# Kernel optimization log

Measured on AMD Instinct MI355X. Metric: run time of the kernel, lower is better.

The kernel has to match this reference:

```python
import jax, jax.numpy as jnp
import numpy as np

TABLE = 4194304   # maxGridFeatId[-1]
D = 4             # eachGridFeatDim
L = 6             # gridFeatLevelCnt (code indexes sigma1..sigma6)
DIR = 16          # in_dim_dir
H = 64            # hidden_dim_color
B, N = 16384, 128


def _linear_init(key, fan_in, fan_out):
    # matches torch nn.Linear default U(-1/sqrt(fan_in), 1/sqrt(fan_in))
    s = 1.0 / np.sqrt(fan_in)
    kw, kb = jax.random.split(key)
    W = jax.random.uniform(kw, (fan_in, fan_out), minval=-s, maxval=s, dtype=jnp.float32)
    b = jax.random.uniform(kb, (fan_out,), minval=-s, maxval=s, dtype=jnp.float32)
    return W, b


def setup_inputs() -> dict:
    key = jax.random.key(0)
    ks = jax.random.split(key, 6)
    x = jax.random.randint(ks[0], (B, N, L), 0, TABLE)
    d = jax.random.normal(ks[1], (B, DIR), dtype=jnp.float32)
    gridWeight = jax.random.uniform(ks[2], (TABLE, D), dtype=jnp.float32)  # torch.rand
    in0 = DIR + L * (D - 1)  # 16 + 18 = 34
    W0, b0 = _linear_init(ks[3], in0, H)
    W1, b1 = _linear_init(ks[4], H, H)
    W2, b2 = _linear_init(ks[5], H, 3)
    return dict(x=x, d=d, gridWeight=gridWeight, W0=W0, b0=b0, W1=W1, b1=b1, W2=W2, b2=b2)


def reference(x, d, gridWeight, W0, b0, W1, b1, W2, b2):
    Bv, Nv, Lv = x.shape
    Dv = gridWeight.shape[-1]
    # embedding gather: (B, N, L, D); same memory order as torch reshape(B, N*L, D)
    feat = gridWeight[x]
    # per-level densities, clipped then multiplied (prod over the 6 levels)
    sig = jnp.clip(feat[..., 0], 0.0, 1.0)                 # (B, N, L)
    sigma0 = jnp.prod(sig, axis=-1, keepdims=True) + 1e-4  # (B, N, 1)
    sigma = sigma0 / jnp.max(sigma0, axis=1, keepdims=True)
    # geometric features: (B, N, L*(D-1))
    geo = feat[..., 1:].reshape(Bv, Nv, Lv * (Dv - 1))
    h = jnp.concatenate([jnp.broadcast_to(d[:, None, :], (Bv, Nv, d.shape[-1])), geo], axis=-1)
    h = jax.nn.relu(h @ W0 + b0)
    h = jax.nn.relu(h @ W1 + b1)
    color = jax.nn.sigmoid(h @ W2 + b2)                    # (B, N, 3)
    # alpha compositing: NOTE original does torch.cumprod(..., dim=2) on a
    # (B, N, 1) tensor, i.e. cumprod over a size-1 axis == identity. Faithful.
    alpha = 1.0 - sigma
    transparentBefore = jnp.concatenate(
        [jnp.ones((Bv, 1, 1), dtype=sigma.dtype), alpha[:, :-1]], axis=1)
    colorWeight0 = transparentBefore * sigma               # (B, N, 1)
    colorOut = colorWeight0 * color                        # (B, N, 3)
    return sigma, jnp.sum(colorOut, axis=1)                # (B,N,1), (B,3)
```

## Files before the change

kernel.cpp:

```cpp
#include <hip/hip_runtime.h>
#include <math.h>


typedef short bf16x8 __attribute__((ext_vector_type(8)));
typedef float floatx4 __attribute__((ext_vector_type(4)));

__device__ inline unsigned short f2b(float f) {
    union { float f; unsigned u; } v; v.f = f;
    unsigned r = v.u + 0x7FFF + ((v.u >> 16) & 1);
    return (unsigned short)(r >> 16);
}

__global__ void build_frags(const float* __restrict__ W0,
                            const float* __restrict__ W1,
                            const float* __restrict__ W2,
                            unsigned short* __restrict__ wsf) {
    int tid = blockIdx.x * blockDim.x + threadIdx.x;
    if (tid >= 7168) return;
    int lane, j, k, n;
    float val;
    if (tid < 2048) {
        int f = tid >> 9, r = tid & 511; lane = r >> 3; j = r & 7;
        k = ((lane >> 4) * 8) + j;
        n = f * 16 + (lane & 15);
        val = (k < 18) ? W0[(16 + k) * 64 + n] : 0.0f;
    } else if (tid < 6144) {
        int e = tid - 2048;
        int f = e >> 9, r = e & 511; lane = r >> 3; j = r & 7;
        int ks = f >> 2, nt = f & 3;
        k = ks * 32 + ((lane >> 4) * 8) + j;
        n = nt * 16 + (lane & 15);
        val = W1[k * 64 + n];
    } else {
        int e = tid - 6144;
        int f = e >> 9, r = e & 511; lane = r >> 3; j = r & 7;
        k = f * 32 + ((lane >> 4) * 8) + j;
        n = lane & 15;
        val = (n < 3) ? W2[k * 3 + n] : 0.0f;
    }
    wsf[tid] = f2b(val);
}

__global__ __launch_bounds__(512, 4) void surf_main(
    const int*   __restrict__ x,
    const float* __restrict__ dvec,
    const float* __restrict__ gw,
    const float* __restrict__ W0,
    const float* __restrict__ b0,
    const float* __restrict__ b1,
    const float* __restrict__ b2,
    const unsigned short* __restrict__ wsf,
    float* __restrict__ out_sigma,
    float* __restrict__ out_color)
{
    const int b    = blockIdx.x;
    const int t    = threadIdx.x;
    const int lane = t & 63;
    const int w    = t >> 6;
    const int l15  = lane & 15;
    const int quad = lane >> 4;

    __shared__ unsigned short A0[128 * 40];
    __shared__ unsigned short H1[128 * 72];
    __shared__ float s_sigl[768];
    __shared__ float s_dirW[64];
    __shared__ float s_wmax[2];
    __shared__ float s_cw[128];
    __shared__ float s_part[8 * 16];

    bf16x8 bw0[4], bw1[8];
    #pragma unroll
    for (int i = 0; i < 4; ++i) bw0[i] = *(const bf16x8*)(wsf + i * 512 + lane * 8);
    #pragma unroll
    for (int i = 0; i < 8; ++i) bw1[i] = *(const bf16x8*)(wsf + 2048 + i * 512 + lane * 8);

    #pragma unroll
    for (int e0 = 0; e0 < 768; e0 += 512) {
        int e = e0 + t;
        if (e < 768) {
            int xv = x[(size_t)b * 768 + e];
            int point = e / 6;
            int level = e - point * 6;
            float4 v = *(const float4*)(gw + (size_t)xv * 4);
            s_sigl[e] = fminf(fmaxf(v.x, 0.0f), 1.0f);
            unsigned short* a = A0 + point * 40 + level * 3;
            a[0] = f2b(v.y); a[1] = f2b(v.z); a[2] = f2b(v.w);
        }
    }
    if (t < 128) {
        unsigned short* a = A0 + t * 40;
        *(unsigned int*)(a + 18) = 0u;
        *(uint2*)(a + 20) = make_uint2(0u, 0u);
        *(uint2*)(a + 24) = make_uint2(0u, 0u);
        *(uint2*)(a + 28) = make_uint2(0u, 0u);
    }
    if (t < 64) {
        float acc = b0[t];
        const float* db = dvec + (size_t)b * 16;
        #pragma unroll
        for (int i = 0; i < 16; ++i) acc = fmaf(db[i], W0[i * 64 + t], acc);
        s_dirW[t] = acc;
    }
    __syncthreads();

    float sigma0 = 0.0f;
    if (t < 128) {
        float p = 1.0f;
        #pragma unroll
        for (int l = 0; l < 6; ++l) p *= s_sigl[t * 6 + l];
        sigma0 = p + 1e-4f;
        float m = sigma0;
        #pragma unroll
        for (int off = 32; off; off >>= 1) m = fmaxf(m, __shfl_xor(m, off));
        if (lane == 0) s_wmax[w] = m;
    }
    __syncthreads();
    if (t < 128) {
        float maxv  = fmaxf(s_wmax[0], s_wmax[1]);
        float sigma = sigma0 / maxv;
        out_sigma[(size_t)b * 128 + t] = sigma;
        float cw;
        if (t == 0) cw = sigma;
        else {
            float pp = 1.0f;
            #pragma unroll
            for (int l = 0; l < 6; ++l) pp *= s_sigl[(t - 1) * 6 + l];
            float sprev = (pp + 1e-4f) / maxv;
            cw = (1.0f - sprev) * sigma;
        }
        s_cw[t] = cw;
    }

    const int row = w * 16 + l15;
    bf16x8 a0 = *(const bf16x8*)(A0 + row * 40 + quad * 8);
    floatx4 acc0[4];
    #pragma unroll
    for (int nt = 0; nt < 4; ++nt) {
        float dw = s_dirW[nt * 16 + l15];
        acc0[nt] = (floatx4){dw, dw, dw, dw};
        acc0[nt] = __builtin_amdgcn_mfma_f32_16x16x32_bf16(a0, bw0[nt], acc0[nt], 0, 0, 0);
    }
    #pragma unroll
    for (int nt = 0; nt < 4; ++nt)
        #pragma unroll
        for (int r = 0; r < 4; ++r) {
            int pr = w * 16 + quad * 4 + r;
            H1[pr * 72 + nt * 16 + l15] = f2b(fmaxf(acc0[nt][r], 0.0f));
        }

    bf16x8 a1a = *(const bf16x8*)(H1 + row * 72 + quad * 8);
    bf16x8 a1b = *(const bf16x8*)(H1 + row * 72 + 32 + quad * 8);
    floatx4 acc1[4];
    #pragma unroll
    for (int nt = 0; nt < 4; ++nt) {
        float bb = b1[nt * 16 + l15];
        acc1[nt] = (floatx4){bb, bb, bb, bb};
        acc1[nt] = __builtin_amdgcn_mfma_f32_16x16x32_bf16(a1a, bw1[nt],     acc1[nt], 0, 0, 0);
        acc1[nt] = __builtin_amdgcn_mfma_f32_16x16x32_bf16(a1b, bw1[4 + nt], acc1[nt], 0, 0, 0);
    }
    #pragma unroll
    for (int nt = 0; nt < 4; ++nt)
        #pragma unroll
        for (int r = 0; r < 4; ++r) {
            int pr = w * 16 + quad * 4 + r;
            H1[pr * 72 + nt * 16 + l15] = f2b(fmaxf(acc1[nt][r], 0.0f));
        }

    bf16x8 bw2a = *(const bf16x8*)(wsf + 6144 + lane * 8);
    bf16x8 bw2b = *(const bf16x8*)(wsf + 6144 + 512 + lane * 8);
    bf16x8 a2a = *(const bf16x8*)(H1 + row * 72 + quad * 8);
    bf16x8 a2b = *(const bf16x8*)(H1 + row * 72 + 32 + quad * 8);
    float bias2 = (l15 < 3) ? b2[l15] : 0.0f;
    floatx4 acc2 = (floatx4){bias2, bias2, bias2, bias2};
    acc2 = __builtin_amdgcn_mfma_f32_16x16x32_bf16(a2a, bw2a, acc2, 0, 0, 0);
    acc2 = __builtin_amdgcn_mfma_f32_16x16x32_bf16(a2b, bw2b, acc2, 0, 0, 0);

    __syncthreads();
    float sum = 0.0f;
    #pragma unroll
    for (int r = 0; r < 4; ++r) {
        float col = 1.0f / (1.0f + __expf(-acc2[r]));
        float cw  = s_cw[w * 16 + quad * 4 + r];
        sum += cw * col;
    }
    sum += __shfl_xor(sum, 16);
    sum += __shfl_xor(sum, 32);
    if (lane < 16) s_part[w * 16 + lane] = sum;
    __syncthreads();
    if (t < 3) {
        float o = 0.0f;
        #pragma unroll
        for (int ww = 0; ww < 8; ++ww) o += s_part[ww * 16 + t];
        out_color[(size_t)b * 3 + t] = o;
    }
}

extern "C" void kernel_launch(void* const* d_in, const int* in_sizes, int n_in,
                              void* d_out, int out_size, void* d_ws, size_t ws_size,
                              hipStream_t stream) {
    const int*   x    = (const int*)d_in[0];
    const float* dvec = (const float*)d_in[1];
    const float* gw   = (const float*)d_in[2];
    const float* W0   = (const float*)d_in[3];
    const float* b0   = (const float*)d_in[4];
    const float* W1   = (const float*)d_in[5];
    const float* b1   = (const float*)d_in[6];
    const float* W2   = (const float*)d_in[7];
    const float* b2   = (const float*)d_in[8];

    const int B = in_sizes[1] / 16;
    float* out_sigma = (float*)d_out;
    float* out_color = (float*)d_out + (size_t)B * 128;
    unsigned short* wsf = (unsigned short*)d_ws;

    build_frags<<<14, 512, 0, stream>>>(W0, W1, W2, wsf);
    surf_main<<<B, 512, 0, stream>>>(x, dvec, gw, W0, b0, b1, b2, wsf,
                                     out_sigma, out_color);
}
```

Before: 336.5 us.

## Process several rays per block with software-pipelined gather prefetch

Each block now handles four rays in a loop instead of one, prefetching the next ray's grid gathers and the following ray's indices while the current ray's MLP runs. Weight fragments are staged once into shared memory per block rather than held in registers, which frees registers so launch bounds can ask for higher occupancy. The aim is to hide the random-gather latency and spread per-block setup over more rays. The cost is more shared-memory traffic for the weight fragments, extra syncs inside the loop, and a grid that is four times smaller.

Measured after the change: 391.2 us. 16.3% more time.

```diff
diff --git a/kernel.cpp b/kernel.cpp
--- a/kernel.cpp
+++ b/kernel.cpp
@@ -1,6 +1,8 @@
 #include <hip/hip_runtime.h>
 #include <math.h>
 
+
+#define RPB 4
 
 typedef short bf16x8 __attribute__((ext_vector_type(8)));
 typedef float floatx4 __attribute__((ext_vector_type(4)));
@@ -41,157 +43,200 @@
     wsf[tid] = f2b(val);
 }
 
-__global__ __launch_bounds__(512, 4) void surf_main(
+__global__ __launch_bounds__(512, 6) void surf_main(
     const int*   __restrict__ x,
     const float* __restrict__ dvec,
     const float* __restrict__ gw,
     const float* __restrict__ W0,
-    const float* __restrict__ b0,
-    const float* __restrict__ b1,
-    const float* __restrict__ b2,
+    const float* __restrict__ b0v,
+    const float* __restrict__ b1v,
+    const float* __restrict__ b2v,
     const unsigned short* __restrict__ wsf,
     float* __restrict__ out_sigma,
     float* __restrict__ out_color)
 {
-    const int b    = blockIdx.x;
     const int t    = threadIdx.x;
     const int lane = t & 63;
     const int w    = t >> 6;
     const int l15  = lane & 15;
     const int quad = lane >> 4;
 
-    __shared__ unsigned short A0[128 * 40];
-    __shared__ unsigned short H1[128 * 72];
+    __shared__ unsigned short UB[128 * 72];
+    __shared__ unsigned short WF[7168];
     __shared__ float s_sigl[768];
     __shared__ float s_dirW[64];
     __shared__ float s_wmax[2];
     __shared__ float s_cw[128];
-    __shared__ float s_part[8 * 16];
-
-    bf16x8 bw0[4], bw1[8];
+    __shared__ float s_part[128];
+
+    const size_t ray0 = (size_t)blockIdx.x * RPB;
+
+    {
+        const unsigned int* src = (const unsigned int*)wsf;
+        unsigned int* dst = (unsigned int*)WF;
+        #pragma unroll
+        for (int i = 0; i < 7; ++i) dst[t + i * 512] = src[t + i * 512];
+    }
+
+    float b1r[4];
     #pragma unroll
-    for (int i = 0; i < 4; ++i) bw0[i] = *(const bf16x8*)(wsf + i * 512 + lane * 8);
+    for (int nt = 0; nt < 4; ++nt) b1r[nt] = b1v[nt * 16 + l15];
+    const float b2r = (l15 < 3) ? b2v[l15] : 0.0f;
+
+    float dwAll[RPB];
+    if (t < 64) {
+        #pragma unroll
+        for (int r = 0; r < RPB; ++r) {
+            float acc = b0v[t];
+            const float* db = dvec + (ray0 + r) * 16;
+            #pragma unroll
+            for (int i = 0; i < 16; ++i) acc = fmaf(db[i], W0[i * 64 + t], acc);
+            dwAll[r] = acc;
+        }
+    }
+
+    const int* xb = x + ray0 * 768;
+    int xq0 = xb[t];
+    int xq1 = (t < 256) ? xb[512 + t] : 0;
+    float4 g0, g1 = make_float4(0.f, 0.f, 0.f, 0.f);
+    g0 = *(const float4*)(gw + (size_t)xq0 * 4);
+    if (t < 256) g1 = *(const float4*)(gw + (size_t)xq1 * 4);
+    {
+        const int* xb1 = x + (ray0 + 1) * 768;
+        xq0 = xb1[t];
+        xq1 = (t < 256) ? xb1[512 + t] : 0;
+    }
+
     #pragma unroll
-    for (int i = 0; i < 8; ++i) bw1[i] = *(const bf16x8*)(wsf + 2048 + i * 512 + lane * 8);
-
-    #pragma unroll
-    for (int e0 = 0; e0 < 768; e0 += 512) {
-        int e = e0 + t;
-        if (e < 768) {
-            int xv = x[(size_t)b * 768 + e];
-            int point = e / 6;
-            int level = e - point * 6;
-            float4 v = *(const float4*)(gw + (size_t)xv * 4);
-            s_sigl[e] = fminf(fmaxf(v.x, 0.0f), 1.0f);
-            unsigned short* a = A0 + point * 40 + level * 3;
-            a[0] = f2b(v.y); a[1] = f2b(v.z); a[2] = f2b(v.w);
-        }
-    }
-    if (t < 128) {
-        unsigned short* a = A0 + t * 40;
-        *(unsigned int*)(a + 18) = 0u;
-        *(uint2*)(a + 20) = make_uint2(0u, 0u);
-        *(uint2*)(a + 24) = make_uint2(0u, 0u);
-        *(uint2*)(a + 28) = make_uint2(0u, 0u);
-    }
-    if (t < 64) {
-        float acc = b0[t];
-        const float* db = dvec + (size_t)b * 16;
-        #pragma unroll
-        for (int i = 0; i < 16; ++i) acc = fmaf(db[i], W0[i * 64 + t], acc);
-        s_dirW[t] = acc;
-    }
-    __syncthreads();
-
-    float sigma0 = 0.0f;
-    if (t < 128) {
-        float p = 1.0f;
-        #pragma unroll
-        for (int l = 0; l < 6; ++l) p *= s_sigl[t * 6 + l];
-        sigma0 = p + 1e-4f;
-        float m = sigma0;
-        #pragma unroll
-        for (int off = 32; off; off >>= 1) m = fmaxf(m, __shfl_xor(m, off));
-        if (lane == 0) s_wmax[w] = m;
-    }
-    __syncthreads();
-    if (t < 128) {
-        float maxv  = fmaxf(s_wmax[0], s_wmax[1]);
-        float sigma = sigma0 / maxv;
-        out_sigma[(size_t)b * 128 + t] = sigma;
-        float cw;
-        if (t == 0) cw = sigma;
-        else {
-            float pp = 1.0f;
-            #pragma unroll
-            for (int l = 0; l < 6; ++l) pp *= s_sigl[(t - 1) * 6 + l];
-            float sprev = (pp + 1e-4f) / maxv;
-            cw = (1.0f - sprev) * sigma;
-        }
-        s_cw[t] = cw;
-    }
-
-    const int row = w * 16 + l15;
-    bf16x8 a0 = *(const bf16x8*)(A0 + row * 40 + quad * 8);
-    floatx4 acc0[4];
-    #pragma unroll
-    for (int nt = 0; nt < 4; ++nt) {
-        float dw = s_dirW[nt * 16 + l15];
-        acc0[nt] = (floatx4){dw, dw, dw, dw};
-        acc0[nt] = __builtin_amdgcn_mfma_f32_16x16x32_bf16(a0, bw0[nt], acc0[nt], 0, 0, 0);
-    }
-    #pragma unroll
-    for (int nt = 0; nt < 4; ++nt)
-        #pragma unroll
-        for (int r = 0; r < 4; ++r) {
-            int pr = w * 16 + quad * 4 + r;
-            H1[pr * 72 + nt * 16 + l15] = f2b(fmaxf(acc0[nt][r], 0.0f));
-        }
-
-    bf16x8 a1a = *(const bf16x8*)(H1 + row * 72 + quad * 8);
-    bf16x8 a1b = *(const bf16x8*)(H1 + row * 72 + 32 + quad * 8);
-    floatx4 acc1[4];
-    #pragma unroll
-    for (int nt = 0; nt < 4; ++nt) {
-        float bb = b1[nt * 16 + l15];
-        acc1[nt] = (floatx4){bb, bb, bb, bb};
-        acc1[nt] = __builtin_amdgcn_mfma_f32_16x16x32_bf16(a1a, bw1[nt],     acc1[nt], 0, 0, 0);
-        acc1[nt] = __builtin_amdgcn_mfma_f32_16x16x32_bf16(a1b, bw1[4 + nt], acc1[nt], 0, 0, 0);
-    }
-    #pragma unroll
-    for (int nt = 0; nt < 4; ++nt)
-        #pragma unroll
-        for (int r = 0; r < 4; ++r) {
-            int pr = w * 16 + quad * 4 + r;
-            H1[pr * 72 + nt * 16 + l15] = f2b(fmaxf(acc1[nt][r], 0.0f));
-        }
-
-    bf16x8 bw2a = *(const bf16x8*)(wsf + 6144 + lane * 8);
-    bf16x8 bw2b = *(const bf16x8*)(wsf + 6144 + 512 + lane * 8);
-    bf16x8 a2a = *(const bf16x8*)(H1 + row * 72 + quad * 8);
-    bf16x8 a2b = *(const bf16x8*)(H1 + row * 72 + 32 + quad * 8);
-    float bias2 = (l15 < 3) ? b2[l15] : 0.0f;
-    floatx4 acc2 = (floatx4){bias2, bias2, bias2, bias2};
-    acc2 = __builtin_amdgcn_mfma_f32_16x16x32_bf16(a2a, bw2a, acc2, 0, 0, 0);
-    acc2 = __builtin_amdgcn_mfma_f32_16x16x32_bf16(a2b, bw2b, acc2, 0, 0, 0);
-
-    __syncthreads();
-    float sum = 0.0f;
-    #pragma unroll
-    for (int r = 0; r < 4; ++r) {
-        float col = 1.0f / (1.0f + __expf(-acc2[r]));
-        float cw  = s_cw[w * 16 + quad * 4 + r];
-        sum += cw * col;
-    }
-    sum += __shfl_xor(sum, 16);
-    sum += __shfl_xor(sum, 32);
-    if (lane < 16) s_part[w * 16 + lane] = sum;
-    __syncthreads();
-    if (t < 3) {
-        float o = 0.0f;
-        #pragma unroll
-        for (int ww = 0; ww < 8; ++ww) o += s_part[ww * 16 + t];
-        out_color[(size_t)b * 3 + t] = o;
+    for (int r = 0; r < RPB; ++r) {
+        const size_t ray = ray0 + r;
+
+        float4 ng0 = make_float4(0.f, 0.f, 0.f, 0.f);
+        float4 ng1 = make_float4(0.f, 0.f, 0.f, 0.f);
+        int nx0 = 0, nx1 = 0;
+        if (r + 1 < RPB) {
+            ng0 = *(const float4*)(gw + (size_t)xq0 * 4);
+            if (t < 256) ng1 = *(const float4*)(gw + (size_t)xq1 * 4);
+            if (r + 2 < RPB) {
+                const int* xb2 = x + (ray + 2) * 768;
+                nx0 = xb2[t];
+                if (t < 256) nx1 = xb2[512 + t];
+            }
+        }
+
+        {
+            int e = t, p = e / 6, li = e - p * 6;
+            s_sigl[e] = fminf(fmaxf(g0.x, 0.0f), 1.0f);
+            unsigned short* a = UB + p * 40 + li * 3;
+            a[0] = f2b(g0.y); a[1] = f2b(g0.z); a[2] = f2b(g0.w);
+        }
+        if (t < 256) {
+            int e = 512 + t, p = e / 6, li = e - p * 6;
+            s_sigl[e] = fminf(fmaxf(g1.x, 0.0f), 1.0f);
+            unsigned short* a = UB + p * 40 + li * 3;
+            a[0] = f2b(g1.y); a[1] = f2b(g1.z); a[2] = f2b(g1.w);
+        }
+        if (t < 128) {
+            unsigned short* a = UB + t * 40;
+            *(unsigned int*)(a + 18) = 0u;
+            *(uint2*)(a + 20) = make_uint2(0u, 0u);
+            *(uint2*)(a + 24) = make_uint2(0u, 0u);
+            *(uint2*)(a + 28) = make_uint2(0u, 0u);
+        }
+        if (t < 64) s_dirW[t] = dwAll[r];
+        __syncthreads();
+
+        float sigma0 = 0.0f;
+        if (t < 128) {
+            float p = 1.0f;
+            #pragma unroll
+            for (int l = 0; l < 6; ++l) p *= s_sigl[t * 6 + l];
+            sigma0 = p + 1e-4f;
+            float m = sigma0;
+            #pragma unroll
+            for (int off = 32; off; off >>= 1) m = fmaxf(m, __shfl_xor(m, off));
+            if (lane == 0) s_wmax[w] = m;
+        }
+        const int row = w * 16 + l15;
+        bf16x8 a0 = *(const bf16x8*)(UB + row * 40 + quad * 8);
+        __syncthreads();
+
+        const float maxv = fmaxf(s_wmax[0], s_wmax[1]);
+        if (t < 128) {
+            float sigma = sigma0 / maxv;
+            out_sigma[ray * 128 + t] = sigma;
+            float cw;
+            if (t == 0) cw = sigma;
+            else {
+                float pp = 1.0f;
+                #pragma unroll
+                for (int l = 0; l < 6; ++l) pp *= s_sigl[(t - 1) * 6 + l];
+                cw = (1.0f - (pp + 1e-4f) / maxv) * sigma;
+            }
+            s_cw[t] = cw;
+        }
+
+        floatx4 acc0[4];
+        #pragma unroll
+        for (int nt = 0; nt < 4; ++nt) {
+            bf16x8 bw = *(const bf16x8*)(WF + nt * 512 + lane * 8);
+            float dw = s_dirW[nt * 16 + l15];
+            acc0[nt] = (floatx4){dw, dw, dw, dw};
+            acc0[nt] = __builtin_amdgcn_mfma_f32_16x16x32_bf16(a0, bw, acc0[nt], 0, 0, 0);
+        }
+        #pragma unroll
+        for (int nt = 0; nt < 4; ++nt)
+            #pragma unroll
+            for (int rr = 0; rr < 4; ++rr)
+                UB[(w * 16 + quad * 4 + rr) * 72 + nt * 16 + l15] =
+                    f2b(fmaxf(acc0[nt][rr], 0.0f));
+
+        bf16x8 a1a = *(const bf16x8*)(UB + row * 72 + quad * 8);
+        bf16x8 a1b = *(const bf16x8*)(UB + row * 72 + 32 + quad * 8);
+        floatx4 acc1[4];
+        #pragma unroll
+        for (int nt = 0; nt < 4; ++nt) {
+            bf16x8 bwa = *(const bf16x8*)(WF + 2048 + nt * 512 + lane * 8);
+            bf16x8 bwb = *(const bf16x8*)(WF + 2048 + (4 + nt) * 512 + lane * 8);
+            float bb = b1r[nt];
+            acc1[nt] = (floatx4){bb, bb, bb, bb};
+            acc1[nt] = __builtin_amdgcn_mfma_f32_16x16x32_bf16(a1a, bwa, acc1[nt], 0, 0, 0);
+            acc1[nt] = __builtin_amdgcn_mfma_f32_16x16x32_bf16(a1b, bwb, acc1[nt], 0, 0, 0);
+        }
+        #pragma unroll
+        for (int nt = 0; nt < 4; ++nt)
+            #pragma unroll
+            for (int rr = 0; rr < 4; ++rr)
+                UB[(w * 16 + quad * 4 + rr) * 72 + nt * 16 + l15] =
+                    f2b(fmaxf(acc1[nt][rr], 0.0f));
+
+        bf16x8 a2a = *(const bf16x8*)(UB + row * 72 + quad * 8);
+        bf16x8 a2b = *(const bf16x8*)(UB + row * 72 + 32 + quad * 8);
+        bf16x8 bw2a = *(const bf16x8*)(WF + 6144 + lane * 8);
+        bf16x8 bw2b = *(const bf16x8*)(WF + 6656 + lane * 8);
+        floatx4 acc2 = (floatx4){b2r, b2r, b2r, b2r};
+        acc2 = __builtin_amdgcn_mfma_f32_16x16x32_bf16(a2a, bw2a, acc2, 0, 0, 0);
+        acc2 = __builtin_amdgcn_mfma_f32_16x16x32_bf16(a2b, bw2b, acc2, 0, 0, 0);
+
+        __syncthreads();
+        float sum = 0.0f;
+        #pragma unroll
+        for (int rr = 0; rr < 4; ++rr) {
+            float col = 1.0f / (1.0f + __expf(-acc2[rr]));
+            sum += s_cw[w * 16 + quad * 4 + rr] * col;
+        }
+        sum += __shfl_xor(sum, 16);
+        sum += __shfl_xor(sum, 32);
+        if (lane < 16) s_part[w * 16 + lane] = sum;
+        __syncthreads();
+        if (t < 3) {
+            float o = 0.0f;
+            #pragma unroll
+            for (int ww = 0; ww < 8; ++ww) o += s_part[ww * 16 + t];
+            out_color[ray * 3 + t] = o;
+        }
+
+        g0 = ng0; g1 = ng1; xq0 = nx0; xq1 = nx1;
     }
 }
 
@@ -214,6 +259,6 @@
     unsigned short* wsf = (unsigned short*)d_ws;
 
     build_frags<<<14, 512, 0, stream>>>(W0, W1, W2, wsf);
-    surf_main<<<B, 512, 0, stream>>>(x, dvec, gw, W0, b0, b1, b2, wsf,
-                                     out_sigma, out_color);
-}
+    surf_main<<<B / RPB, 512, 0, stream>>>(x, dvec, gw, W0, b0, b1, b2, wsf,
+                                           out_sigma, out_color);
+}
```

## Map one wavefront per ray and loop MLP tiles without block barriers

Applied to the files above, without the earlier changes.

Restructures the main kernel so each 64-lane wavefront owns a whole ray (128 points), with 4 rays per 256-thread block, instead of one ray per 512-thread block. Each lane gathers 12 table rows (two full points) with vectorized index loads, computes sigma, the max reduction and the compositing weights entirely in registers via wave shuffles, and packs bf16 features with wide LDS stores. The MLP then loops over 8 row tiles per wave with a per-wave scratch buffer, removing all __syncthreads and the cross-wave reductions. The trade-off is fewer gather loads in flight per thread-slot, serialized MFMA work per wave, and a larger shared-memory footprint per block, which may reduce occupancy.

After: 349.7 us. 3.9% more time.

```diff
diff --git a/kernel.cpp b/kernel.cpp
--- a/kernel.cpp
+++ b/kernel.cpp
@@ -1,4 +1,5 @@
 #include <hip/hip_runtime.h>
+#include <hip/hip_bf16.h>
 #include <math.h>
 
 
@@ -9,6 +10,9 @@
     union { float f; unsigned u; } v; v.f = f;
     unsigned r = v.u + 0x7FFF + ((v.u >> 16) & 1);
     return (unsigned short)(r >> 16);
+}
+__device__ inline unsigned pk2(float a, float b) {
+    return (unsigned)f2b(a) | ((unsigned)f2b(b) << 16);
 }
 
 __global__ void build_frags(const float* __restrict__ W0,
@@ -41,158 +45,168 @@
     wsf[tid] = f2b(val);
 }
 
-__global__ __launch_bounds__(512, 4) void surf_main(
+__global__ __launch_bounds__(256) void surf_main(
     const int*   __restrict__ x,
     const float* __restrict__ dvec,
     const float* __restrict__ gw,
     const float* __restrict__ W0,
-    const float* __restrict__ b0,
-    const float* __restrict__ b1,
-    const float* __restrict__ b2,
+    const float* __restrict__ b0v,
+    const float* __restrict__ b1v,
+    const float* __restrict__ b2v,
     const unsigned short* __restrict__ wsf,
     float* __restrict__ out_sigma,
     float* __restrict__ out_color)
 {
-    const int b    = blockIdx.x;
     const int t    = threadIdx.x;
     const int lane = t & 63;
     const int w    = t >> 6;
     const int l15  = lane & 15;
     const int quad = lane >> 4;
-
-    __shared__ unsigned short A0[128 * 40];
-    __shared__ unsigned short H1[128 * 72];
-    __shared__ float s_sigl[768];
-    __shared__ float s_dirW[64];
-    __shared__ float s_wmax[2];
-    __shared__ float s_cw[128];
-    __shared__ float s_part[8 * 16];
-
-    bf16x8 bw0[4], bw1[8];
+    const size_t ray = (size_t)blockIdx.x * 4 + w;
+
+    __shared__ unsigned short A0[4][128 * 40];
+    __shared__ unsigned short HT[4][16 * 72];
+    __shared__ float cwL[4][128];
+    __shared__ float dwL[4][64];
+
+    unsigned short* A0w = A0[w];
+    unsigned short* HTw = HT[w];
+    float* cww = cwL[w];
+    float* dww = dwL[w];
+
+    const int* xp = x + ray * 768 + lane * 12;
+    const int4 xa = *(const int4*)(xp);
+    const int4 xb = *(const int4*)(xp + 4);
+    const int4 xc = *(const int4*)(xp + 8);
+
+    float4 g[12];
+    g[0]  = *(const float4*)(gw + (size_t)xa.x * 4);
+    g[1]  = *(const float4*)(gw + (size_t)xa.y * 4);
+    g[2]  = *(const float4*)(gw + (size_t)xa.z * 4);
+    g[3]  = *(const float4*)(gw + (size_t)xa.w * 4);
+    g[4]  = *(const float4*)(gw + (size_t)xb.x * 4);
+    g[5]  = *(const float4*)(gw + (size_t)xb.y * 4);
+    g[6]  = *(const float4*)(gw + (size_t)xb.z * 4);
+    g[7]  = *(const float4*)(gw + (size_t)xb.w * 4);
+    g[8]  = *(const float4*)(gw + (size_t)xc.x * 4);
+    g[9]  = *(const float4*)(gw + (size_t)xc.y * 4);
+    g[10] = *(const float4*)(gw + (size_t)xc.z * 4);
+    g[11] = *(const float4*)(gw + (size_t)xc.w * 4);
+
+    {
+        float acc = b0v[lane];
+        const float* db = dvec + ray * 16;
+        #pragma unroll
+        for (int i = 0; i < 16; ++i) acc = fmaf(db[i], W0[i * 64 + lane], acc);
+        dww[lane] = acc;
+    }
+
+    float sig0[2];
+    #pragma unroll
+    for (int p = 0; p < 2; ++p) {
+        const float4* gp = g + 6 * p;
+        float s = 1.0f;
+        #pragma unroll
+        for (int l = 0; l < 6; ++l)
+            s *= fminf(fmaxf(gp[l].x, 0.0f), 1.0f);
+        sig0[p] = s + 1e-4f;
+        unsigned u0 = pk2(gp[0].y, gp[0].z);
+        unsigned u1 = pk2(gp[0].w, gp[1].y);
+        unsigned u2 = pk2(gp[1].z, gp[1].w);
+        unsigned u3 = pk2(gp[2].y, gp[2].z);
+        unsigned u4 = pk2(gp[2].w, gp[3].y);
+        unsigned u5 = pk2(gp[3].z, gp[3].w);
+        unsigned u6 = pk2(gp[4].y, gp[4].z);
+        unsigned u7 = pk2(gp[4].w, gp[5].y);
+        unsigned u8 = pk2(gp[5].z, gp[5].w);
+        int4* dst = (int4*)(A0w + (lane * 2 + p) * 40);
+        dst[0] = make_int4((int)u0, (int)u1, (int)u2, (int)u3);
+        dst[1] = make_int4((int)u4, (int)u5, (int)u6, (int)u7);
+        dst[2] = make_int4((int)u8, 0, 0, 0);
+        dst[3] = make_int4(0, 0, 0, 0);
+    }
+
+    float m = fmaxf(sig0[0], sig0[1]);
+    #pragma unroll
+    for (int off = 1; off < 64; off <<= 1)
+        m = fmaxf(m, __shfl_xor(m, off));
+    const float sp0 = sig0[0] / m;
+    const float sp1 = sig0[1] / m;
+    {
+        float2 sv; sv.x = sp0; sv.y = sp1;
+        *(float2*)(out_sigma + ray * 128 + lane * 2) = sv;
+    }
+    const float prev = __shfl_up(sp1, 1);
+    const float cw0 = (lane == 0) ? sp0 : (1.0f - prev) * sp0;
+    const float cw1 = (1.0f - sp0) * sp1;
+    {
+        float2 cv; cv.x = cw0; cv.y = cw1;
+        *(float2*)(cww + lane * 2) = cv;
+    }
+
+    bf16x8 bw0[4], bw1[8], bw2[2];
     #pragma unroll
     for (int i = 0; i < 4; ++i) bw0[i] = *(const bf16x8*)(wsf + i * 512 + lane * 8);
     #pragma unroll
     for (int i = 0; i < 8; ++i) bw1[i] = *(const bf16x8*)(wsf + 2048 + i * 512 + lane * 8);
-
-    #pragma unroll
-    for (int e0 = 0; e0 < 768; e0 += 512) {
-        int e = e0 + t;
-        if (e < 768) {
-            int xv = x[(size_t)b * 768 + e];
-            int point = e / 6;
-            int level = e - point * 6;
-            float4 v = *(const float4*)(gw + (size_t)xv * 4);
-            s_sigl[e] = fminf(fmaxf(v.x, 0.0f), 1.0f);
-            unsigned short* a = A0 + point * 40 + level * 3;
-            a[0] = f2b(v.y); a[1] = f2b(v.z); a[2] = f2b(v.w);
+    bw2[0] = *(const bf16x8*)(wsf + 6144 + lane * 8);
+    bw2[1] = *(const bf16x8*)(wsf + 6656 + lane * 8);
+    float b1r[4];
+    #pragma unroll
+    for (int nt = 0; nt < 4; ++nt) b1r[nt] = b1v[nt * 16 + l15];
+    const float b2r = (l15 < 3) ? b2v[l15] : 0.0f;
+    float dw4[4];
+    #pragma unroll
+    for (int nt = 0; nt < 4; ++nt) dw4[nt] = dww[nt * 16 + l15];
+
+    float csum = 0.0f;
+    for (int mt = 0; mt < 8; ++mt) {
+        bf16x8 a0 = *(const bf16x8*)(A0w + (mt * 16 + l15) * 40 + quad * 8);
+
+        floatx4 acc0[4];
+        #pragma unroll
+        for (int nt = 0; nt < 4; ++nt) {
+            float dw = dw4[nt];
+            acc0[nt] = (floatx4){dw, dw, dw, dw};
+            acc0[nt] = __builtin_amdgcn_mfma_f32_16x16x32_bf16(a0, bw0[nt], acc0[nt], 0, 0, 0);
         }
-    }
-    if (t < 128) {
-        unsigned short* a = A0 + t * 40;
-        *(unsigned int*)(a + 18) = 0u;
-        *(uint2*)(a + 20) = make_uint2(0u, 0u);
-        *(uint2*)(a + 24) = make_uint2(0u, 0u);
-        *(uint2*)(a + 28) = make_uint2(0u, 0u);
-    }
-    if (t < 64) {
-        float acc = b0[t];
-        const float* db = dvec + (size_t)b * 16;
-        #pragma unroll
-        for (int i = 0; i < 16; ++i) acc = fmaf(db[i], W0[i * 64 + t], acc);
-        s_dirW[t] = acc;
-    }
-    __syncthreads();
-
-    float sigma0 = 0.0f;
-    if (t < 128) {
-        float p = 1.0f;
-        #pragma unroll
-        for (int l = 0; l < 6; ++l) p *= s_sigl[t * 6 + l];
-        sigma0 = p + 1e-4f;
-        float m = sigma0;
-        #pragma unroll
-        for (int off = 32; off; off >>= 1) m = fmaxf(m, __shfl_xor(m, off));
-        if (lane == 0) s_wmax[w] = m;
-    }
-    __syncthreads();
-    if (t < 128) {
-        float maxv  = fmaxf(s_wmax[0], s_wmax[1]);
-        float sigma = sigma0 / maxv;
-        out_sigma[(size_t)b * 128 + t] = sigma;
-        float cw;
-        if (t == 0) cw = sigma;
-        else {
-            float pp = 1.0f;
+        #pragma unroll
+        for (int nt = 0; nt < 4; ++nt)
             #pragma unroll
-            for (int l = 0; l < 6; ++l) pp *= s_sigl[(t - 1) * 6 + l];
-            float sprev = (pp + 1e-4f) / maxv;
-            cw = (1.0f - sprev) * sigma;
+            for (int r = 0; r < 4; ++r)
+                HTw[(quad * 4 + r) * 72 + nt * 16 + l15] = f2b(fmaxf(acc0[nt][r], 0.0f));
+
+        bf16x8 a1a = *(const bf16x8*)(HTw + l15 * 72 + quad * 8);
+        bf16x8 a1b = *(const bf16x8*)(HTw + l15 * 72 + 32 + quad * 8);
+        floatx4 acc1[4];
+        #pragma unroll
+        for (int nt = 0; nt < 4; ++nt) {
+            float bb = b1r[nt];
+            acc1[nt] = (floatx4){bb, bb, bb, bb};
+            acc1[nt] = __builtin_amdgcn_mfma_f32_16x16x32_bf16(a1a, bw1[nt],     acc1[nt], 0, 0, 0);
+            acc1[nt] = __builtin_amdgcn_mfma_f32_16x16x32_bf16(a1b, bw1[4 + nt], acc1[nt], 0, 0, 0);
         }
-        s_cw[t] = cw;
-    }
-
-    const int row = w * 16 + l15;
-    bf16x8 a0 = *(const bf16x8*)(A0 + row * 40 + quad * 8);
-    floatx4 acc0[4];
-    #pragma unroll
-    for (int nt = 0; nt < 4; ++nt) {
-        float dw = s_dirW[nt * 16 + l15];
-        acc0[nt] = (floatx4){dw, dw, dw, dw};
-        acc0[nt] = __builtin_amdgcn_mfma_f32_16x16x32_bf16(a0, bw0[nt], acc0[nt], 0, 0, 0);
-    }
-    #pragma unroll
-    for (int nt = 0; nt < 4; ++nt)
-        #pragma unroll
-        for (int r = 0; r < 4; ++r) {
-            int pr = w * 16 + quad * 4 + r;
-            H1[pr * 72 + nt * 16 + l15] = f2b(fmaxf(acc0[nt][r], 0.0f));
-        }
-
-    bf16x8 a1a = *(const bf16x8*)(H1 + row * 72 + quad * 8);
-    bf16x8 a1b = *(const bf16x8*)(H1 + row * 72 + 32 + quad * 8);
-    floatx4 acc1[4];
-    #pragma unroll
-    for (int nt = 0; nt < 4; ++nt) {
-        float bb = b1[nt * 16 + l15];
-        acc1[nt] = (floatx4){bb, bb, bb, bb};
-        acc1[nt] = __builtin_amdgcn_mfma_f32_16x16x32_bf16(a1a, bw1[nt],     acc1[nt], 0, 0, 0);
-        acc1[nt] = __builtin_amdgcn_mfma_f32_16x16x32_bf16(a1b, bw1[4 + nt], acc1[nt], 0, 0, 0);
-    }
-    #pragma unroll
-    for (int nt = 0; nt < 4; ++nt)
-        #pragma unroll
-        for (int r = 0; r < 4; ++r) {
-            int pr = w * 16 + quad * 4 + r;
-            H1[pr * 72 + nt * 16 + l15] = f2b(fmaxf(acc1[nt][r], 0.0f));
-        }
-
-    bf16x8 bw2a = *(const bf16x8*)(wsf + 6144 + lane * 8);
-    bf16x8 bw2b = *(const bf16x8*)(wsf + 6144 + 512 + lane * 8);
-    bf16x8 a2a = *(const bf16x8*)(H1 + row * 72 + quad * 8);
-    bf16x8 a2b = *(const bf16x8*)(H1 + row * 72 + 32 + quad * 8);
-    float bias2 = (l15 < 3) ? b2[l15] : 0.0f;
-    floatx4 acc2 = (floatx4){bias2, bias2, bias2, bias2};
-    acc2 = __builtin_amdgcn_mfma_f32_16x16x32_bf16(a2a, bw2a, acc2, 0, 0, 0);
-    acc2 = __builtin_amdgcn_mfma_f32_16x16x32_bf16(a2b, bw2b, acc2, 0, 0, 0);
-
-    __syncthreads();
-    float sum = 0.0f;
-    #pragma unroll
-    for (int r = 0; r < 4; ++r) {
-        float col = 1.0f / (1.0f + __expf(-acc2[r]));
-        float cw  = s_cw[w * 16 + quad * 4 + r];
-        sum += cw * col;
-    }
-    sum += __shfl_xor(sum, 16);
-    sum += __shfl_xor(sum, 32);
-    if (lane < 16) s_part[w * 16 + lane] = sum;
-    __syncthreads();
-    if (t < 3) {
-        float o = 0.0f;
-        #pragma unroll
-        for (int ww = 0; ww < 8; ++ww) o += s_part[ww * 16 + t];
-        out_color[(size_t)b * 3 + t] = o;
-    }
+        #pragma unroll
+        for (int nt = 0; nt < 4; ++nt)
+            #pragma unroll
+            for (int r = 0; r < 4; ++r)
+                HTw[(quad * 4 + r) * 72 + nt * 16 + l15] = f2b(fmaxf(acc1[nt][r], 0.0f));
+
+        bf16x8 a2a = *(const bf16x8*)(HTw + l15 * 72 + quad * 8);
+        bf16x8 a2b = *(const bf16x8*)(HTw + l15 * 72 + 32 + quad * 8);
+        floatx4 acc2 = (floatx4){b2r, b2r, b2r, b2r};
+        acc2 = __builtin_amdgcn_mfma_f32_16x16x32_bf16(a2a, bw2[0], acc2, 0, 0, 0);
+        acc2 = __builtin_amdgcn_mfma_f32_16x16x32_bf16(a2b, bw2[1], acc2, 0, 0, 0);
+
+        floatx4 cwq = *(const floatx4*)(cww + mt * 16 + quad * 4);
+        #pragma unroll
+        for (int r = 0; r < 4; ++r)
+            csum += cwq[r] / (1.0f + __expf(-acc2[r]));
+    }
+
+    csum += __shfl_xor(csum, 16);
+    csum += __shfl_xor(csum, 32);
+    if (lane < 3) out_color[ray * 3 + lane] = csum;
 }
 
 extern "C" void kernel_launch(void* const* d_in, const int* in_sizes, int n_in,
@@ -214,6 +228,6 @@
     unsigned short* wsf = (unsigned short*)d_ws;
 
     build_frags<<<14, 512, 0, stream>>>(W0, W1, W2, wsf);
-    surf_main<<<B, 512, 0, stream>>>(x, dvec, gw, W0, b0, b1, b2, wsf,
-                                     out_sigma, out_color);
-}
+    surf_main<<<B / 4, 256, 0, stream>>>(x, dvec, gw, W0, b0, b1, b2, wsf,
+                                         out_sigma, out_color);
+}
```
